# Performance work log

Measured on AMD Instinct MI355X. Metric: run time of the kernel, lower is better.

Reference implementation:

```python
import jax, jax.numpy as jnp
import numpy as np

B, S, H = 2, 2048, 2048
NH = 16
HD = H // NH
SCALE = 1.0 / float(np.sqrt(HD))


def setup_inputs() -> dict:
    key = jax.random.key(0)
    ks = jax.random.split(key, 4)
    x = jax.random.normal(ks[0], (B, S, H), dtype=jnp.float32)
    # causal mask: 1 = attend, 0 = masked (masked_fill where mask == 0)
    attn_mask = jnp.tril(jnp.ones((S, S), dtype=jnp.int32))[None, None, :, :]
    w_qkv = jax.random.normal(ks[1], (3 * H, H), dtype=jnp.float32) * (1.0 / np.sqrt(H))
    b_qkv = jnp.zeros((3 * H,), dtype=jnp.float32)
    w_out = jax.random.normal(ks[2], (H, H), dtype=jnp.float32) * (1.0 / np.sqrt(H))
    b_out = jnp.zeros((H,), dtype=jnp.float32)
    return {"x": x, "attn_mask": attn_mask, "w_qkv": w_qkv, "b_qkv": b_qkv,
            "w_out": w_out, "b_out": b_out}


def reference(x, attn_mask, w_qkv, b_qkv, w_out, b_out):
    bsz, seq_len, hidden = x.shape
    # qkv projection (torch Linear: x @ W.T + b); TP gather is identity on 1 device
    qkv = jnp.einsum('bsh,oh->bso', x, w_qkv) + b_qkv  # [B,S,3H]
    q, k, v = jnp.split(qkv, 3, axis=-1)
    def shape(t):  # [B,S,H] -> [B,NH,S,HD]
        return t.reshape(bsz, seq_len, NH, HD).transpose(0, 2, 1, 3)
    q, k, v = shape(q), shape(k), shape(v)
    attn = jnp.einsum('bhqd,bhkd->bhqk', q, k) * SCALE  # [B,NH,S,S]
    attn = jnp.where(attn_mask == 0, jnp.float32(-10000.0), attn)
    attn = jax.nn.softmax(attn, axis=-1)  # dropout_p = 0 -> identity
    ctx = jnp.einsum('bhqk,bhkd->bhqd', attn, v)
    ctx = ctx.transpose(0, 2, 1, 3).reshape(bsz, seq_len, hidden)
    out = jnp.einsum('bsh,oh->bso', ctx, w_out) + b_out
    return out
```

## Files before the change

kernel.cpp:

```cpp
#include <hip/hip_runtime.h>
#include <hip/hip_bf16.h>
#include <stdint.h>

#define B_ 2
#define S_ 2048
#define H_ 2048
#define NH_ 16
#define HD_ 128
#define SCALE_ 0.08838834764831845f
#define QSCALE_ 0.12751743558230564f

typedef __attribute__((ext_vector_type(8))) short bf16x8;
typedef __attribute__((ext_vector_type(4))) float f32x4;

__device__ __forceinline__ unsigned short f2bf(float f) {
  union { float f; unsigned int u; } c;
  c.f = f;
  unsigned int u = c.u;
  unsigned int r = (u + 0x7fffu + ((u >> 16) & 1u)) >> 16;
  return (unsigned short)r;
}

__global__ void cvt_f32_bf16_k(const float* __restrict__ in,
                               unsigned short* __restrict__ out, int n4) {
  int i = blockIdx.x * blockDim.x + threadIdx.x;
  if (i < n4) {
    float4 v = reinterpret_cast<const float4*>(in)[i];
    ushort4 o;
    o.x = f2bf(v.x); o.y = f2bf(v.y); o.z = f2bf(v.z); o.w = f2bf(v.w);
    reinterpret_cast<ushort4*>(out)[i] = o;
  }
}

template <int MODE>
__global__ __launch_bounds__(256) void gemm_bt_k(
    const unsigned short* __restrict__ A,
    const unsigned short* __restrict__ Bm,
    const float* __restrict__ bias,
    int K, int N,
    float* __restrict__ outf,
    unsigned short* __restrict__ Qp,
    unsigned short* __restrict__ Kp,
    unsigned short* __restrict__ Vn) {
  __shared__ unsigned short Al[128 * 32];
  __shared__ unsigned short Bl[128 * 32];
  const int tid = threadIdx.x;
  const int lane = tid & 63;
  const int w = tid >> 6;
  const int wr = w >> 1, wc = w & 1;
  const int brow = blockIdx.y * 128, bcol = blockIdx.x * 128;
  const int lr = lane & 15, lg = lane >> 4;
  f32x4 acc[4][4] = {};

  for (int kb = 0; kb < K; kb += 32) {
    __syncthreads();
#pragma unroll
    for (int p = 0; p < 2; ++p) {
      int c = p * 256 + tid;
      int row = c >> 2, kc = (c & 3) * 8;
      __builtin_amdgcn_global_load_lds(
          (const __attribute__((address_space(1))) unsigned int*)(A + (size_t)(brow + row) * K + kb + kc),
          (__attribute__((address_space(3))) unsigned int*)(Al + c * 8), 16, 0, 0);
      __builtin_amdgcn_global_load_lds(
          (const __attribute__((address_space(1))) unsigned int*)(Bm + (size_t)(bcol + row) * K + kb + kc),
          (__attribute__((address_space(3))) unsigned int*)(Bl + c * 8), 16, 0, 0);
    }
    __syncthreads();
    bf16x8 af[4], bfr[4];
#pragma unroll
    for (int m = 0; m < 4; ++m)
      af[m] = *reinterpret_cast<const bf16x8*>(&Al[(wr * 64 + m * 16 + lr) * 32 + lg * 8]);
#pragma unroll
    for (int n = 0; n < 4; ++n)
      bfr[n] = *reinterpret_cast<const bf16x8*>(&Bl[(wc * 64 + n * 16 + lr) * 32 + lg * 8]);
#pragma unroll
    for (int m = 0; m < 4; ++m)
#pragma unroll
      for (int n = 0; n < 4; ++n)
        acc[m][n] = __builtin_amdgcn_mfma_f32_16x16x32_bf16(af[m], bfr[n], acc[m][n], 0, 0, 0);
  }

#pragma unroll
  for (int m = 0; m < 4; ++m) {
#pragma unroll
    for (int n = 0; n < 4; ++n) {
      int gcol = bcol + wc * 64 + n * 16 + lr;
      int grow0 = brow + wr * 64 + m * 16 + lg * 4;
      float bv = bias[gcol];
      if (MODE == 1) {
#pragma unroll
        for (int r = 0; r < 4; ++r)
          outf[(size_t)(grow0 + r) * N + gcol] = acc[m][n][r] + bv;
      } else {
        int region = gcol >> 11;
        int o = gcol & 2047;
        int head = o >> 7, d = o & 127;
#pragma unroll
        for (int r = 0; r < 4; ++r) {
          int grow = grow0 + r;
          int b = grow >> 11, s = grow & 2047;
          float fv = acc[m][n][r] + bv;
          if (region == 0)
            Qp[((size_t)(b * NH_ + head) * S_ + s) * HD_ + d] = f2bf(fv * QSCALE_);
          else if (region == 1)
            Kp[((size_t)(b * NH_ + head) * S_ + s) * HD_ + d] = f2bf(fv);
          else
            Vn[(size_t)grow * H_ + o] = f2bf(fv);
        }
      }
    }
  }
}

__global__ void transpose_v_k(const unsigned short* __restrict__ Vn,
                              unsigned short* __restrict__ Vt) {
  __shared__ unsigned short t[32][33];
  int bh = blockIdx.z;
  int b = bh >> 4, h = bh & 15;
  int s0 = blockIdx.x * 32, d0 = blockIdx.y * 32;
  int x = threadIdx.x, y0 = threadIdx.y;
#pragma unroll
  for (int yy = 0; yy < 32; yy += 8) {
    int s = s0 + y0 + yy;
    t[y0 + yy][x] = Vn[((size_t)(b * S_ + s)) * H_ + h * HD_ + d0 + x];
  }
  __syncthreads();
#pragma unroll
  for (int yy = 0; yy < 32; yy += 8) {
    int d = d0 + y0 + yy;
    Vt[((size_t)(bh * HD_ + d)) * S_ + s0 + x] = t[x][y0 + yy];
  }
}

__global__ __launch_bounds__(512, 4) void flash_attn_k(
    const unsigned short* __restrict__ Qp,
    const unsigned short* __restrict__ Kp,
    const unsigned short* __restrict__ Vt,
    unsigned short* __restrict__ ctx) {
  __shared__ unsigned short Kl[64 * 128];
  __shared__ unsigned short Vl[128 * 64];
  __shared__ unsigned short Pl[8][16 * 72];

  const int tid = threadIdx.x;
  const int lane = tid & 63, w = tid >> 6;
  const int lr = lane & 15, lg = lane >> 4;
  const int bid = blockIdx.x;
  const int bh = bid & 31;
  const int qi = 15 - (bid >> 5);
  const int b = bh >> 4, h = bh & 15;
  const int qtile = qi * 128;
  const int qbase = qtile + w * 16;

  const unsigned short* Qh = Qp + (size_t)bh * S_ * HD_;
  const unsigned short* Kh = Kp + (size_t)bh * S_ * HD_;
  const unsigned short* Vh = Vt + (size_t)bh * HD_ * S_;

  bf16x8 qf[4];
#pragma unroll
  for (int dc = 0; dc < 4; ++dc)
    qf[dc] = *reinterpret_cast<const bf16x8*>(Qh + (size_t)(qbase + lr) * HD_ + dc * 32 + lg * 8);

  f32x4 acc_o[8] = {};
  float m_r[4], l_r[4];
#pragma unroll
  for (int r = 0; r < 4; ++r) { m_r[r] = -1e30f; l_r[r] = 0.f; }

  const int nkb = 2 * qi + 2;
  for (int kb = 0; kb < nkb; ++kb) {
    __syncthreads();
    const unsigned short* Kbase = Kh + (size_t)(kb * 64) * HD_;
    const unsigned short* Vbase = Vh + kb * 64;
#pragma unroll
    for (int c2 = 0; c2 < 2; ++c2) {
      int chunk = c2 * 512 + tid;
      int krow = chunk >> 4;
      int kcol = (chunk & 15) << 4;
      int kswz = kcol ^ ((krow & 7) << 4);
      __builtin_amdgcn_global_load_lds(
          (const __attribute__((address_space(1))) unsigned int*)(Kbase + krow * HD_ + (kswz >> 1)),
          (__attribute__((address_space(3))) unsigned int*)(Kl + chunk * 8), 16, 0, 0);
      int vrow = chunk >> 3;
      int vcol = (chunk & 7) << 4;
      int vswz = vcol ^ ((vrow & 7) << 4);
      __builtin_amdgcn_global_load_lds(
          (const __attribute__((address_space(1))) unsigned int*)(Vbase + (size_t)vrow * S_ + (vswz >> 1)),
          (__attribute__((address_space(3))) unsigned int*)(Vl + chunk * 8), 16, 0, 0);
    }
    __syncthreads();

    f32x4 sa[4] = {};
#pragma unroll
    for (int n = 0; n < 4; ++n) {
      int row = n * 16 + lr;
#pragma unroll
      for (int dc = 0; dc < 4; ++dc) {
        int byte = row * 256 + dc * 64 + lg * 16;
        byte ^= (row & 7) << 4;
        bf16x8 kf = *reinterpret_cast<const bf16x8*>(
            reinterpret_cast<const char*>(Kl) + byte);
        sa[n] = __builtin_amdgcn_mfma_f32_16x16x32_bf16(qf[dc], kf, sa[n], 0, 0, 0);
      }
    }

    if (kb * 64 + 63 > qbase) {
#pragma unroll
      for (int n = 0; n < 4; ++n) {
        int col = kb * 64 + n * 16 + lr;
#pragma unroll
        for (int r = 0; r < 4; ++r) {
          int rowq = qbase + lg * 4 + r;
          if (col > rowq) sa[n][r] = -1e30f;
        }
      }
    }
#pragma unroll
    for (int r = 0; r < 4; ++r) {
      float mx = fmaxf(fmaxf(sa[0][r], sa[1][r]), fmaxf(sa[2][r], sa[3][r]));
#pragma unroll
      for (int off = 1; off < 16; off <<= 1)
        mx = fmaxf(mx, __shfl_xor(mx, off));
      float mnew = fmaxf(m_r[r], mx);
      float alpha = exp2f(m_r[r] - mnew);
      float rs = 0.f;
#pragma unroll
      for (int n = 0; n < 4; ++n) {
        float p = exp2f(sa[n][r] - mnew);
        rs += p;
        Pl[w][(lg * 4 + r) * 72 + n * 16 + lr] = f2bf(p);
      }
#pragma unroll
      for (int off = 1; off < 16; off <<= 1)
        rs += __shfl_xor(rs, off);
      l_r[r] = l_r[r] * alpha + rs;
      m_r[r] = mnew;
#pragma unroll
      for (int nc = 0; nc < 8; ++nc)
        acc_o[nc][r] *= alpha;
    }

    bf16x8 pa[2];
#pragma unroll
    for (int ks = 0; ks < 2; ++ks)
      pa[ks] = *reinterpret_cast<const bf16x8*>(&Pl[w][lr * 72 + ks * 32 + lg * 8]);
#pragma unroll
    for (int nc = 0; nc < 8; ++nc) {
      int row = nc * 16 + lr;
#pragma unroll
      for (int ks = 0; ks < 2; ++ks) {
        int byte = row * 128 + ks * 64 + lg * 16;
        byte ^= (row & 7) << 4;
        bf16x8 vf = *reinterpret_cast<const bf16x8*>(
            reinterpret_cast<const char*>(Vl) + byte);
        acc_o[nc] = __builtin_amdgcn_mfma_f32_16x16x32_bf16(pa[ks], vf, acc_o[nc], 0, 0, 0);
      }
    }
  }

#pragma unroll
  for (int nc = 0; nc < 8; ++nc) {
#pragma unroll
    for (int r = 0; r < 4; ++r) {
      int s = qbase + lg * 4 + r;
      float v = acc_o[nc][r] / l_r[r];
      ctx[((size_t)(b * S_ + s)) * H_ + h * HD_ + nc * 16 + lr] = f2bf(v);
    }
  }
}

extern "C" void kernel_launch(void* const* d_in, const int* in_sizes, int n_in,
                              void* d_out, int out_size, void* d_ws, size_t ws_size,
                              hipStream_t stream) {
  const float* x = (const float*)d_in[0];
  const float* w_qkv = (const float*)d_in[2];
  const float* b_qkv = (const float*)d_in[3];
  const float* w_out = (const float*)d_in[4];
  const float* b_out = (const float*)d_in[5];
  float* out = (float*)d_out;

  char* ws = (char*)d_ws;
  unsigned short* xb    = (unsigned short*)(ws);
  unsigned short* wqkvb = (unsigned short*)(ws + 16777216);
  unsigned short* woutb = (unsigned short*)(ws + 41943040);
  unsigned short* Qp    = (unsigned short*)(ws + 50331648);
  unsigned short* Kp    = (unsigned short*)(ws + 67108864);
  unsigned short* Vn    = (unsigned short*)(ws + 83886080);
  unsigned short* Vt    = (unsigned short*)(ws + 100663296);
  unsigned short* ctx   = (unsigned short*)(ws + 117440512);

  hipLaunchKernelGGL(cvt_f32_bf16_k, dim3(8192), dim3(256), 0, stream, x, xb, 2097152);
  hipLaunchKernelGGL(cvt_f32_bf16_k, dim3(12288), dim3(256), 0, stream, w_qkv, wqkvb, 3145728);
  hipLaunchKernelGGL(cvt_f32_bf16_k, dim3(4096), dim3(256), 0, stream, w_out, woutb, 1048576);

  hipLaunchKernelGGL((gemm_bt_k<0>), dim3(48, 32), dim3(256), 0, stream,
                     xb, wqkvb, b_qkv, 2048, 6144, (float*)nullptr, Qp, Kp, Vn);

  hipLaunchKernelGGL(transpose_v_k, dim3(64, 4, 32), dim3(32, 8), 0, stream, Vn, Vt);

  hipLaunchKernelGGL(flash_attn_k, dim3(512), dim3(512), 0, stream, Qp, Kp, Vt, ctx);

  hipLaunchKernelGGL((gemm_bt_k<1>), dim3(16, 32), dim3(256), 0, stream,
                     ctx, woutb, b_out, 2048, 2048, out,
                     (unsigned short*)nullptr, (unsigned short*)nullptr, (unsigned short*)nullptr);
}
```

Baseline: 498.6 us.

## Transpose QK^T MFMA layout to cut softmax shuffles and skip fully-masked blocks

Swaps the MFMA operand order so each lane holds one query row's scores across four key columns. The row max and sum then need two cross-lane shuffles instead of four per row, and one m/l value per lane instead of four. P is packed to bf16 with v_cvt_pk_bf16_f32 and written as 8-byte stores. Per-warp key blocks lying entirely above the causal diagonal skip compute, and the final divide becomes a multiply by a shuffled reciprocal. The cost is extra __shfl broadcasts of alpha and 1/l to the output layout, plus a warp-divergent branch inside a block-synchronous loop.

```diff
diff --git a/kernel.cpp b/kernel.cpp
--- a/kernel.cpp
+++ b/kernel.cpp
@@ -19,6 +19,12 @@
   unsigned int u = c.u;
   unsigned int r = (u + 0x7fffu + ((u >> 16) & 1u)) >> 16;
   return (unsigned short)r;
+}
+
+__device__ __forceinline__ unsigned int cvt_pk_bf16(float lo, float hi) {
+  unsigned int r;
+  asm("v_cvt_pk_bf16_f32 %0, %1, %2" : "=v"(r) : "v"(lo), "v"(hi));
+  return r;
 }
 
 __global__ void cvt_f32_bf16_k(const float* __restrict__ in,
@@ -161,9 +167,7 @@
     qf[dc] = *reinterpret_cast<const bf16x8*>(Qh + (size_t)(qbase + lr) * HD_ + dc * 32 + lg * 8);
 
   f32x4 acc_o[8] = {};
-  float m_r[4], l_r[4];
-#pragma unroll
-  for (int r = 0; r < 4; ++r) { m_r[r] = -1e30f; l_r[r] = 0.f; }
+  float m_r = -1e30f, l_r = 0.f;
 
   const int nkb = 2 * qi + 2;
   for (int kb = 0; kb < nkb; ++kb) {
@@ -188,81 +192,106 @@
     }
     __syncthreads();
 
-    f32x4 sa[4] = {};
-#pragma unroll
-    for (int n = 0; n < 4; ++n) {
-      int row = n * 16 + lr;
-#pragma unroll
-      for (int dc = 0; dc < 4; ++dc) {
-        int byte = row * 256 + dc * 64 + lg * 16;
-        byte ^= (row & 7) << 4;
-        bf16x8 kf = *reinterpret_cast<const bf16x8*>(
-            reinterpret_cast<const char*>(Kl) + byte);
-        sa[n] = __builtin_amdgcn_mfma_f32_16x16x32_bf16(qf[dc], kf, sa[n], 0, 0, 0);
-      }
-    }
-
-    if (kb * 64 + 63 > qbase) {
+    const bool live = (kb * 64 <= qbase + 15);
+    if (live) {
+      f32x4 sa[4] = {};
 #pragma unroll
       for (int n = 0; n < 4; ++n) {
-        int col = kb * 64 + n * 16 + lr;
-#pragma unroll
-        for (int r = 0; r < 4; ++r) {
-          int rowq = qbase + lg * 4 + r;
-          if (col > rowq) sa[n][r] = -1e30f;
+        int row = n * 16 + lr;
+#pragma unroll
+        for (int dc = 0; dc < 4; ++dc) {
+          int byte = row * 256 + dc * 64 + lg * 16;
+          byte ^= (row & 7) << 4;
+          bf16x8 kf = *reinterpret_cast<const bf16x8*>(
+              reinterpret_cast<const char*>(Kl) + byte);
+          sa[n] = __builtin_amdgcn_mfma_f32_16x16x32_bf16(kf, qf[dc], sa[n], 0, 0, 0);
         }
       }
-    }
-#pragma unroll
-    for (int r = 0; r < 4; ++r) {
-      float mx = fmaxf(fmaxf(sa[0][r], sa[1][r]), fmaxf(sa[2][r], sa[3][r]));
-#pragma unroll
-      for (int off = 1; off < 16; off <<= 1)
-        mx = fmaxf(mx, __shfl_xor(mx, off));
-      float mnew = fmaxf(m_r[r], mx);
-      float alpha = exp2f(m_r[r] - mnew);
-      float rs = 0.f;
+
+      if (kb * 64 + 63 > qbase) {
+        int rowq = qbase + lr;
+#pragma unroll
+        for (int n = 0; n < 4; ++n) {
+          int col0 = kb * 64 + n * 16 + lg * 4;
+#pragma unroll
+          for (int r = 0; r < 4; ++r)
+            if (col0 + r > rowq) sa[n][r] = -1e30f;
+        }
+      }
+
+      float mx4[4];
+#pragma unroll
+      for (int n = 0; n < 4; ++n)
+        mx4[n] = fmaxf(fmaxf(sa[n][0], sa[n][1]), fmaxf(sa[n][2], sa[n][3]));
+      float mx = fmaxf(fmaxf(mx4[0], mx4[1]), fmaxf(mx4[2], mx4[3]));
+      mx = fmaxf(mx, __shfl_xor(mx, 16));
+      mx = fmaxf(mx, __shfl_xor(mx, 32));
+      float mnew = fmaxf(m_r, mx);
+      float alpha = exp2f(m_r - mnew);
+
+      float p[4][4];
+      float rsn[4];
 #pragma unroll
       for (int n = 0; n < 4; ++n) {
-        float p = exp2f(sa[n][r] - mnew);
-        rs += p;
-        Pl[w][(lg * 4 + r) * 72 + n * 16 + lr] = f2bf(p);
-      }
-#pragma unroll
-      for (int off = 1; off < 16; off <<= 1)
-        rs += __shfl_xor(rs, off);
-      l_r[r] = l_r[r] * alpha + rs;
-      m_r[r] = mnew;
+#pragma unroll
+        for (int r = 0; r < 4; ++r)
+          p[n][r] = exp2f(sa[n][r] - mnew);
+        rsn[n] = (p[n][0] + p[n][1]) + (p[n][2] + p[n][3]);
+      }
+      float rs = (rsn[0] + rsn[1]) + (rsn[2] + rsn[3]);
+      rs += __shfl_xor(rs, 16);
+      rs += __shfl_xor(rs, 32);
+      l_r = l_r * alpha + rs;
+      m_r = mnew;
+
+#pragma unroll
+      for (int n = 0; n < 4; ++n) {
+        uint2 pk;
+        pk.x = cvt_pk_bf16(p[n][0], p[n][1]);
+        pk.y = cvt_pk_bf16(p[n][2], p[n][3]);
+        *reinterpret_cast<uint2*>(&Pl[w][lr * 72 + n * 16 + lg * 4]) = pk;
+      }
+
+      float al[4];
+#pragma unroll
+      for (int r = 0; r < 4; ++r)
+        al[r] = __shfl(alpha, lg * 4 + r);
 #pragma unroll
       for (int nc = 0; nc < 8; ++nc)
-        acc_o[nc][r] *= alpha;
-    }
-
-    bf16x8 pa[2];
-#pragma unroll
-    for (int ks = 0; ks < 2; ++ks)
-      pa[ks] = *reinterpret_cast<const bf16x8*>(&Pl[w][lr * 72 + ks * 32 + lg * 8]);
-#pragma unroll
-    for (int nc = 0; nc < 8; ++nc) {
-      int row = nc * 16 + lr;
-#pragma unroll
-      for (int ks = 0; ks < 2; ++ks) {
-        int byte = row * 128 + ks * 64 + lg * 16;
-        byte ^= (row & 7) << 4;
-        bf16x8 vf = *reinterpret_cast<const bf16x8*>(
-            reinterpret_cast<const char*>(Vl) + byte);
-        acc_o[nc] = __builtin_amdgcn_mfma_f32_16x16x32_bf16(pa[ks], vf, acc_o[nc], 0, 0, 0);
-      }
-    }
-  }
-
+#pragma unroll
+        for (int r = 0; r < 4; ++r)
+          acc_o[nc][r] *= al[r];
+
+      bf16x8 pa[2];
+#pragma unroll
+      for (int ks = 0; ks < 2; ++ks)
+        pa[ks] = *reinterpret_cast<const bf16x8*>(&Pl[w][lr * 72 + ks * 32 + lg * 8]);
+#pragma unroll
+      for (int nc = 0; nc < 8; ++nc) {
+        int row = nc * 16 + lr;
+#pragma unroll
+        for (int ks = 0; ks < 2; ++ks) {
+          int byte = row * 128 + ks * 64 + lg * 16;
+          byte ^= (row & 7) << 4;
+          bf16x8 vf = *reinterpret_cast<const bf16x8*>(
+              reinterpret_cast<const char*>(Vl) + byte);
+          acc_o[nc] = __builtin_amdgcn_mfma_f32_16x16x32_bf16(pa[ks], vf, acc_o[nc], 0, 0, 0);
+        }
+      }
+    }
+  }
+
+  float linv = 1.f / l_r;
+  float li[4];
+#pragma unroll
+  for (int r = 0; r < 4; ++r)
+    li[r] = __shfl(linv, lg * 4 + r);
 #pragma unroll
   for (int nc = 0; nc < 8; ++nc) {
 #pragma unroll
     for (int r = 0; r < 4; ++r) {
       int s = qbase + lg * 4 + r;
-      float v = acc_o[nc][r] / l_r[r];
-      ctx[((size_t)(b * S_ + s)) * H_ + h * HD_ + nc * 16 + lr] = f2bf(v);
+      ctx[((size_t)(b * S_ + s)) * H_ + h * HD_ + nc * 16 + lr] = f2bf(acc_o[nc][r] * li[r]);
     }
   }
 }
```

Result: faster. 457.8 us (-8.2%).
